# Kernel optimization log

Measured on AMD Instinct MI355X. Metric: run time of the kernel, lower is better.

Reference implementation:

```python
import jax, jax.numpy as jnp
import numpy as np

N_HEADS = 16
D_HEAD = 64
D_MODEL = 1024
CHUNK = 64
SCALE = 1.0 / np.sqrt(D_HEAD).astype(np.float32)


def binarize(x):
    # {-1,+1} with straight-through gradient (identity in bwd)
    return x + jax.lax.stop_gradient(jnp.where(x >= 0, 1.0, -1.0).astype(x.dtype) - x)


def setup_inputs() -> dict:
    key = jax.random.key(0)
    k1, k2, k3 = jax.random.split(key, 3)
    B, T, D = 2, 4096, D_MODEL
    x = jax.random.normal(k1, (B, T, D), dtype=jnp.float32)
    w_qkv = jax.random.normal(k2, (3 * D, D), dtype=jnp.float32) * (1.0 / np.sqrt(D))
    w_o = jax.random.normal(k3, (D, D), dtype=jnp.float32) * (1.0 / np.sqrt(D))
    return {"x": x, "w_qkv": w_qkv, "w_o": w_o}


def reference(x, w_qkv, w_o):
    B, T, D = x.shape
    H, d, C = N_HEADS, D_HEAD, CHUNK
    qkv = (x @ w_qkv.T).reshape(B, T, 3, H, d)
    q, k, v = qkv[:, :, 0], qkv[:, :, 1], qkv[:, :, 2]
    # -> (B, H, T, d)
    q = jnp.transpose(q, (0, 2, 1, 3)) * jnp.asarray(SCALE, x.dtype)
    k = binarize(jnp.transpose(k, (0, 2, 1, 3)))
    v = binarize(jnp.transpose(v, (0, 2, 1, 3)))

    assert T % C == 0  # T=4096 divisible by chunk=64 (pad branch not exercised)
    Nc = T // C
    qc = q.reshape(B, H, Nc, C, d)
    kc = k.reshape(B, H, Nc, C, d)
    vc = v.reshape(B, H, Nc, C, d)

    causal_mask = jnp.tril(jnp.ones((C, C), dtype=x.dtype))
    # intra-chunk: (B,H,N,C,C) scores, causal-masked, times values
    intra_scores = jnp.einsum('bhnid,bhnjd->bhnij', qc, kc) * causal_mask
    intra = jnp.einsum('bhnij,bhnjd->bhnid', intra_scores, vc)
    # per-chunk KV outer-product state: (B,H,N,d,d)
    chunk_kv = jnp.einsum('bhntk,bhntv->bhnkv', kc, vc)
    prefix = jnp.cumsum(chunk_kv, axis=2) - chunk_kv  # exclusive prefix
    cross = jnp.einsum('bhnck,bhnkv->bhncv', qc, prefix)
    output = (intra + cross).reshape(B, H, T, d)

    final_state = prefix[:, :, -1] + chunk_kv[:, :, -1]
    out = jnp.transpose(output, (0, 2, 1, 3)).reshape(B, T, D)
    return out @ w_o.T, final_state
```

## Files before the change

### kernel.cpp

```cpp
#include <hip/hip_runtime.h>

typedef __bf16 bf16;
typedef __bf16 bf16x8 __attribute__((ext_vector_type(8)));
typedef _Float16 f16;
typedef _Float16 f16x8 __attribute__((ext_vector_type(8)));
typedef float f32x4 __attribute__((ext_vector_type(4)));
typedef short s16x8 __attribute__((ext_vector_type(8)));

#define SCALE 0.125f
#define AP 72
#define CT 128

__device__ __forceinline__ void async_ld16(const void* g, void* l) {
  __builtin_amdgcn_global_load_lds((const __attribute__((address_space(1))) void*)g,
                                   (__attribute__((address_space(3))) void*)l, 16, 0, 0);
}

__global__ __launch_bounds__(256) void k_convert(
    const float* __restrict__ x, const float* __restrict__ wqkv, const float* __restrict__ wo,
    bf16* __restrict__ xsplit, bf16* __restrict__ wsplit, f16* __restrict__ wo16)
{
  const int N1 = 2097152, N2 = 786432, N3 = 262144;
  const int i = blockIdx.x * 256 + threadIdx.x;
  if (i < N1) {
    f32x4 v = ((const f32x4*)x)[i];
    int e = i * 4, m = e >> 10, c = e & 1023;
    bf16 hi[4], lo[4];
#pragma unroll
    for (int u = 0; u < 4; ++u) { hi[u] = (bf16)v[u]; lo[u] = (bf16)(v[u] - (float)hi[u]); }
    *(ulong1*)&xsplit[(size_t)m * 2048 + c] = *(ulong1*)hi;
    *(ulong1*)&xsplit[(size_t)m * 2048 + 1024 + c] = *(ulong1*)lo;
  } else if (i < N1 + N2) {
    int j = i - N1;
    f32x4 v = ((const f32x4*)wqkv)[j];
    int e = j * 4, n = e >> 10, c = e & 1023;
    bf16 hi[4], lo[4];
#pragma unroll
    for (int u = 0; u < 4; ++u) { hi[u] = (bf16)v[u]; lo[u] = (bf16)(v[u] - (float)hi[u]); }
    *(ulong1*)&wsplit[(size_t)n * 2048 + c] = *(ulong1*)hi;
    *(ulong1*)&wsplit[(size_t)n * 2048 + 1024 + c] = *(ulong1*)lo;
  } else if (i < N1 + N2 + N3) {
    int j = i - N1 - N2;
    f32x4 v = ((const f32x4*)wo)[j];
    f16 h[4];
#pragma unroll
    for (int u = 0; u < 4; ++u) h[u] = (f16)v[u];
    *(ulong1*)&wo16[(size_t)j * 4] = *(ulong1*)h;
  }
}

__global__ __launch_bounds__(256) void k_gemm_qkv(
    const bf16* __restrict__ A, const bf16* __restrict__ B,
    bf16* __restrict__ Qws, bf16* __restrict__ Kws, bf16* __restrict__ Vws)
{
  __shared__ char smem[32768];
  const int tid = threadIdx.x;
  const int wave = tid >> 6, lane = tid & 63;
  const int quad = lane >> 4, l16 = lane & 15;
  const int bxr = (blockIdx.x < 16) ? (blockIdx.x + 8) : (blockIdx.x - 16);
  const int n0 = bxr * 128;
  const int m0 = blockIdx.y * 128;
  const int wm = (wave >> 1) << 6, wn = (wave & 1) << 6;
  const int region = n0 >> 10;
  f32x4 acc[4][4] = {};

  if (region == 0) {
    bf16* As = (bf16*)smem;
    bf16* Bs = As + 128 * 64;
    const int r8 = lane >> 3, c8 = lane & 7;
    const int sw = l16 & 7;
    const int srcoff = (c8 ^ r8) * 8;
    for (int k0 = 0; k0 < 1024; k0 += 64) {
      __syncthreads();
#pragma unroll
      for (int it = 0; it < 4; ++it) {
        const int row = wave * 32 + it * 8 + r8;
        async_ld16(A + (size_t)(m0 + row) * 2048 + k0 + srcoff, As + row * 64 + c8 * 8);
        async_ld16(B + (size_t)(n0 + row) * 2048 + k0 + srcoff, Bs + row * 64 + c8 * 8);
      }
      __syncthreads();
#pragma unroll
      for (int ks = 0; ks < 64; ks += 32) {
        bf16x8 af[4], bg[4];
#pragma unroll
        for (int mi = 0; mi < 4; ++mi)
          af[mi] = *(const bf16x8*)&As[(wm + mi * 16 + l16) * 64 + ((((ks >> 3) + quad) ^ sw) << 3)];
#pragma unroll
        for (int ni = 0; ni < 4; ++ni)
          bg[ni] = *(const bf16x8*)&Bs[(wn + ni * 16 + l16) * 64 + ((((ks >> 3) + quad) ^ sw) << 3)];
#pragma unroll
        for (int mi = 0; mi < 4; ++mi)
#pragma unroll
          for (int ni = 0; ni < 4; ++ni)
            acc[mi][ni] = __builtin_amdgcn_mfma_f32_16x16x32_bf16(af[mi], bg[ni], acc[mi][ni], 0, 0, 0);
      }
    }
  } else {
    bf16* Ah = (bf16*)smem;
    bf16* Al = Ah + 128 * 32;
    bf16* Bh = Al + 128 * 32;
    bf16* Bl = Bh + 128 * 32;
    const int rr0 = tid >> 2;
    const int sl = tid & 3;
    const int rsw = quad ^ ((l16 >> 1) & 3);
    for (int k0 = 0; k0 < 1024; k0 += 32) {
      __syncthreads();
#pragma unroll
      for (int rr = 0; rr < 2; ++rr) {
        const int row = rr * 64 + rr0;
        const int soff = ((sl ^ ((row >> 1) & 3)) << 3);
        const bf16* arow = A + (size_t)(m0 + row) * 2048 + k0 + soff;
        const bf16* brow = B + (size_t)(n0 + row) * 2048 + k0 + soff;
        async_ld16(arow,        Ah + row * 32 + sl * 8);
        async_ld16(arow + 1024, Al + row * 32 + sl * 8);
        async_ld16(brow,        Bh + row * 32 + sl * 8);
        async_ld16(brow + 1024, Bl + row * 32 + sl * 8);
      }
      __syncthreads();
#pragma unroll
      for (int cb = 0; cb < 3; ++cb) {
        const bf16* Asrc = (cb == 1) ? Al : Ah;
        const bf16* Bsrc = (cb == 2) ? Bl : Bh;
        bf16x8 af[4], bg[4];
#pragma unroll
        for (int mi = 0; mi < 4; ++mi)
          af[mi] = *(const bf16x8*)&Asrc[(wm + mi * 16 + l16) * 32 + (rsw << 3)];
#pragma unroll
        for (int ni = 0; ni < 4; ++ni)
          bg[ni] = *(const bf16x8*)&Bsrc[(wn + ni * 16 + l16) * 32 + (rsw << 3)];
#pragma unroll
        for (int mi = 0; mi < 4; ++mi)
#pragma unroll
          for (int ni = 0; ni < 4; ++ni)
            acc[mi][ni] = __builtin_amdgcn_mfma_f32_16x16x32_bf16(af[mi], bg[ni], acc[mi][ni], 0, 0, 0);
      }
    }
  }

  bf16* Ct = (bf16*)smem;
  __syncthreads();
#pragma unroll
  for (int mi = 0; mi < 4; ++mi) {
    const int ml = wm + mi * 16 + quad * 4;
#pragma unroll
    for (int ni = 0; ni < 4; ++ni) {
      const int nl = wn + ni * 16 + l16;
#pragma unroll
      for (int r = 0; r < 4; ++r) {
        const float v = acc[mi][ni][r];
        bf16 o;
        if (region == 0) o = (bf16)(v * SCALE);
        else             o = (bf16)((v >= 0.f) ? 1.f : -1.f);
        Ct[(ml + r) * CT + nl] = o;
      }
    }
  }
  __syncthreads();
  {
    const int row = tid >> 1, half = tid & 1;
    const int nn = (n0 & 1023) + half * 64;
    const int h = nn >> 6;
    const int b = m0 >> 12, t = (m0 & 4095) + row;
    bf16* base = (region == 0) ? Qws : (region == 1) ? Kws : Vws;
    bf16* dst = base + ((size_t)(b * 16 + h) * 4096 + t) * 64;
    const bf16* src = &Ct[row * CT + half * 64];
#pragma unroll
    for (int u = 0; u < 8; ++u)
      *(bf16x8*)(dst + u * 8) = *(const bf16x8*)(src + u * 8);
  }
}

__global__ __launch_bounds__(256) void k_ckv(
    const bf16* __restrict__ Kws, const bf16* __restrict__ Vws, short* __restrict__ ckv)
{
  __shared__ bf16 Kt[64 * AP];
  __shared__ bf16 Vt[64 * AP];
  const int tid = threadIdx.x;
  const int nchunk = blockIdx.x & 63, bh = blockIdx.x >> 6;
  const size_t tbase = ((size_t)bh * 4096 + (size_t)nchunk * 64) * 64;
  const int row = tid >> 2, c0 = (tid & 3) << 4;
  {
    const bf16x8* gk = (const bf16x8*)(Kws + tbase + row * 64 + c0);
    const bf16x8* gv = (const bf16x8*)(Vws + tbase + row * 64 + c0);
    bf16x8 k0 = gk[0], k1 = gk[1], v0 = gv[0], v1 = gv[1];
#pragma unroll
    for (int u = 0; u < 8; ++u) {
      Kt[(c0 + u) * AP + row] = k0[u];
      Kt[(c0 + 8 + u) * AP + row] = k1[u];
      Vt[(c0 + u) * AP + row] = v0[u];
      Vt[(c0 + 8 + u) * AP + row] = v1[u];
    }
  }
  __syncthreads();
  const int wave = tid >> 6, lane = tid & 63;
  const int quad = lane >> 4, l16 = lane & 15;
  const int ti = wave;
  bf16x8 ka[2];
#pragma unroll
  for (int kk = 0; kk < 2; ++kk)
    ka[kk] = *(const bf16x8*)&Kt[(ti * 16 + l16) * AP + kk * 32 + quad * 8];
  short* dst = ckv + ((size_t)bh * 64 + nchunk) * 4096;
#pragma unroll
  for (int td = 0; td < 4; ++td) {
    f32x4 acc = {};
#pragma unroll
    for (int kk = 0; kk < 2; ++kk) {
      const bf16x8 vb = *(const bf16x8*)&Vt[(td * 16 + l16) * AP + kk * 32 + quad * 8];
      acc = __builtin_amdgcn_mfma_f32_16x16x32_bf16(ka[kk], vb, acc, 0, 0, 0);
    }
#pragma unroll
    for (int r = 0; r < 4; ++r)
      dst[(ti * 16 + quad * 4 + r) * 64 + td * 16 + l16] = (short)acc[r];
  }
}

__global__ __launch_bounds__(256) void k_scan(short* __restrict__ ckv, float* __restrict__ fin)
{
  const int idx2 = blockIdx.x * 256 + threadIdx.x;
  short* p = ckv + ((size_t)(idx2 >> 11)) * 262144 + (size_t)(idx2 & 2047) * 2;
  int r0 = 0, r1 = 0;
#pragma unroll
  for (int n = 0; n < 64; ++n) {
    unsigned int w = *(unsigned int*)(p + (size_t)n * 4096);
    const short a = (short)(w & 0xffff);
    const short bb = (short)(w >> 16);
    *(unsigned int*)(p + (size_t)n * 4096) =
        ((unsigned int)(unsigned short)(short)r0) | (((unsigned int)(unsigned short)(short)r1) << 16);
    r0 += a; r1 += bb;
  }
  float2 f; f.x = (float)r0; f.y = (float)r1;
  *(float2*)(fin + ((size_t)(idx2 >> 11)) * 4096 + (size_t)(idx2 & 2047) * 2) = f;
}

__global__ __launch_bounds__(256) void k_attn(
    const bf16* __restrict__ Qws, const bf16* __restrict__ Kws, const bf16* __restrict__ Vws,
    const short* __restrict__ pref, f16* __restrict__ attn)
{
  __shared__ bf16 Ks[64 * 64];
  __shared__ bf16 Vt[64 * AP];
  __shared__ bf16 Ph[64 * AP];
  __shared__ bf16 Pl[64 * AP];
  __shared__ bf16 Ss[64 * AP];
  const int tid = threadIdx.x;
  const int nchunk = blockIdx.x & 63, bh = blockIdx.x >> 6;
  const int b = bh >> 4, h = bh & 15;
  const size_t tbase = ((size_t)bh * 4096 + (size_t)nchunk * 64) * 64;

  {
    const int c8 = tid & 7, r0 = tid >> 3;
#pragma unroll
    for (int it = 0; it < 2; ++it) {
      const int row = it * 32 + r0;
      async_ld16(Kws + tbase + row * 64 + ((c8 ^ (row & 7)) << 3), Ks + row * 64 + (c8 << 3));
    }
  }
  const int wave = tid >> 6, lane = tid & 63;
  const int quad = lane >> 4, l16 = lane & 15;
  const int ti = wave;
  bf16x8 qa[2];
#pragma unroll
  for (int kk = 0; kk < 2; ++kk)
    qa[kk] = *(const bf16x8*)(Qws + tbase + (ti * 16 + l16) * 64 + kk * 32 + quad * 8);
  {
    const int row = tid >> 2, c0 = (tid & 3) << 4;
    const bf16x8* gv = (const bf16x8*)(Vws + tbase + row * 64 + c0);
    bf16x8 v0 = gv[0], v1 = gv[1];
#pragma unroll
    for (int u = 0; u < 8; ++u) {
      Vt[(c0 + u) * AP + row] = v0[u];
      Vt[(c0 + 8 + u) * AP + row] = v1[u];
    }
    const short* gp = pref + ((size_t)bh * 64 + nchunk) * 4096 + row * 64 + c0;
    s16x8 p0 = *(const s16x8*)(gp);
    s16x8 p1 = *(const s16x8*)(gp + 8);
#pragma unroll
    for (int u = 0; u < 8; ++u) {
      {
        const float p = (float)p0[u];
        const bf16 hi = (bf16)p;
        Ph[(c0 + u) * AP + row] = hi;
        Pl[(c0 + u) * AP + row] = (bf16)(p - (float)hi);
      }
      {
        const float p = (float)p1[u];
        const bf16 hi = (bf16)p;
        Ph[(c0 + 8 + u) * AP + row] = hi;
        Pl[(c0 + 8 + u) * AP + row] = (bf16)(p - (float)hi);
      }
    }
  }
  __syncthreads();

  const int sw = l16 & 7;
  f32x4 sacc[4] = {};
#pragma unroll
  for (int tj = 0; tj < 4; ++tj)
#pragma unroll
    for (int kk = 0; kk < 2; ++kk) {
      const bf16x8 kb = *(const bf16x8*)&Ks[(tj * 16 + l16) * 64 + (((kk * 4 + quad) ^ sw) << 3)];
      sacc[tj] = __builtin_amdgcn_mfma_f32_16x16x32_bf16(qa[kk], kb, sacc[tj], 0, 0, 0);
    }
#pragma unroll
  for (int tj = 0; tj < 4; ++tj)
#pragma unroll
    for (int r = 0; r < 4; ++r) {
      const int i = ti * 16 + quad * 4 + r;
      const int jj = tj * 16 + l16;
      Ss[i * AP + jj] = (bf16)((jj <= i) ? sacc[tj][r] : 0.f);
    }
  __syncthreads();

  bf16x8 sa[2];
#pragma unroll
  for (int kk = 0; kk < 2; ++kk)
    sa[kk] = *(const bf16x8*)&Ss[(ti * 16 + l16) * AP + kk * 32 + quad * 8];
  f32x4 oacc[4] = {};
#pragma unroll
  for (int td = 0; td < 4; ++td) {
#pragma unroll
    for (int kk = 0; kk < 2; ++kk) {
      const bf16x8 vb = *(const bf16x8*)&Vt[(td * 16 + l16) * AP + kk * 32 + quad * 8];
      oacc[td] = __builtin_amdgcn_mfma_f32_16x16x32_bf16(sa[kk], vb, oacc[td], 0, 0, 0);
    }
#pragma unroll
    for (int kk = 0; kk < 2; ++kk) {
      const bf16x8 pb = *(const bf16x8*)&Ph[(td * 16 + l16) * AP + kk * 32 + quad * 8];
      oacc[td] = __builtin_amdgcn_mfma_f32_16x16x32_bf16(qa[kk], pb, oacc[td], 0, 0, 0);
      const bf16x8 pb2 = *(const bf16x8*)&Pl[(td * 16 + l16) * AP + kk * 32 + quad * 8];
      oacc[td] = __builtin_amdgcn_mfma_f32_16x16x32_bf16(qa[kk], pb2, oacc[td], 0, 0, 0);
    }
  }
  __syncthreads();
  f16* Os = (f16*)Ss;
#pragma unroll
  for (int td = 0; td < 4; ++td)
#pragma unroll
    for (int r = 0; r < 4; ++r) {
      const int i = ti * 16 + quad * 4 + r;
      const int dd = td * 16 + l16;
      Os[i * AP + dd] = (f16)oacc[td][r];
    }
  __syncthreads();
  {
    const int i2 = tid >> 2, q4 = tid & 3;
    const int t = nchunk * 64 + i2;
    f16* dst = attn + ((size_t)(b * 4096 + t)) * 1024 + h * 64 + q4 * 16;
    const f16* src = &Os[i2 * AP + q4 * 16];
    *(f16x8*)(dst) = *(const f16x8*)(src);
    *(f16x8*)(dst + 8) = *(const f16x8*)(src + 8);
  }
}

__global__ __launch_bounds__(256) void k_gemm_out(
    const f16* __restrict__ A, const f16* __restrict__ B, float* __restrict__ out)
{
  __shared__ f16 As[128 * 64];
  __shared__ f16 Bs[128 * 64];
  const int tid = threadIdx.x;
  const int wave = tid >> 6, lane = tid & 63;
  const int quad = lane >> 4, l16 = lane & 15;
  const int n0 = blockIdx.x * 128;
  const int m0 = blockIdx.y * 128;
  const int wm = (wave >> 1) << 6, wn = (wave & 1) << 6;
  const int r8 = lane >> 3, c8 = lane & 7;
  const int sw = l16 & 7;
  const int srcoff = (c8 ^ r8) * 8;
  f32x4 acc[4][4] = {};

  for (int k0 = 0; k0 < 1024; k0 += 64) {
    __syncthreads();
#pragma unroll
    for (int it = 0; it < 4; ++it) {
      const int row = wave * 32 + it * 8 + r8;
      async_ld16(A + (size_t)(m0 + row) * 1024 + k0 + srcoff, As + row * 64 + c8 * 8);
      async_ld16(B + (size_t)(n0 + row) * 1024 + k0 + srcoff, Bs + row * 64 + c8 * 8);
    }
    __syncthreads();
#pragma unroll
    for (int ks = 0; ks < 64; ks += 32) {
      f16x8 af[4], bg[4];
#pragma unroll
      for (int mi = 0; mi < 4; ++mi)
        af[mi] = *(const f16x8*)&As[(wm + mi * 16 + l16) * 64 + ((((ks >> 3) + quad) ^ sw) << 3)];
#pragma unroll
      for (int ni = 0; ni < 4; ++ni)
        bg[ni] = *(const f16x8*)&Bs[(wn + ni * 16 + l16) * 64 + ((((ks >> 3) + quad) ^ sw) << 3)];
#pragma unroll
      for (int mi = 0; mi < 4; ++mi)
#pragma unroll
        for (int ni = 0; ni < 4; ++ni)
          acc[mi][ni] = __builtin_amdgcn_mfma_f32_16x16x32_f16(af[mi], bg[ni], acc[mi][ni], 0, 0, 0);
    }
  }
#pragma unroll
  for (int mi = 0; mi < 4; ++mi)
#pragma unroll
    for (int ni = 0; ni < 4; ++ni)
#pragma unroll
      for (int r = 0; r < 4; ++r) {
        const int m = m0 + wm + mi * 16 + quad * 4 + r;
        const int n = n0 + wn + ni * 16 + l16;
        out[(size_t)m * 1024 + n] = acc[mi][ni][r];
      }
}

extern "C" void kernel_launch(void* const* d_in, const int* in_sizes, int n_in,
                              void* d_out, int out_size, void* d_ws, size_t ws_size,
                              hipStream_t stream)
{
  const float* x = (const float*)d_in[0];
  const float* wqkv = (const float*)d_in[1];
  const float* wo = (const float*)d_in[2];
  float* out = (float*)d_out;
  char* ws = (char*)d_ws;

  bf16* xsplit = (bf16*)(ws);
  bf16* wsplit = (bf16*)(ws + 33554432);
  f16*  wo16   = (f16*)(ws + 46137344);
  bf16* Qws    = (bf16*)(ws + 48234496);
  bf16* Kws    = (bf16*)(ws + 65011712);
  bf16* Vws    = (bf16*)(ws + 81788928);
  short* ckv   = (short*)(ws + 98566144);
  f16*  attn   = (f16*)(ws + 132120576);
  float* fin   = out + 8388608;

  k_convert<<<12288, 256, 0, stream>>>(x, wqkv, wo, xsplit, wsplit, wo16);
  k_gemm_qkv<<<dim3(24, 64), 256, 0, stream>>>(xsplit, wsplit, Qws, Kws, Vws);
  k_ckv<<<2048, 256, 0, stream>>>(Kws, Vws, ckv);
  k_scan<<<256, 256, 0, stream>>>(ckv, fin);
  k_attn<<<2048, 256, 0, stream>>>(Qws, Kws, Vws, ckv, attn);
  k_gemm_out<<<dim3(8, 64), 256, 0, stream>>>(attn, wo16, out);
}
```

Before: 285.3 us.

## Rewrite QKV GEMM as 256x256 8-wave kernel with double-buffered async staging

Replaces the 128x128, 4-wave QKV GEMM with a 256x256-tile, 512-thread kernel. It double-buffers A and B in 128 KB of dynamic LDS, interleaves async global-to-LDS loads with MFMA phases, and uses s_setprio and explicit vmcnt waits to overlap loading with compute. The split-bf16 K/V path becomes a single 48-step loop whose k index wraps to form the hi*hi, lo*hi and hi*lo products. Q blocks take 16 steps and K/V blocks 48, all in one flat grid. The aim is more operand reuse per loaded byte and hidden load latency. The cost is heavy LDS use that limits occupancy to one block per CU, plus uneven block lengths between the Q and K/V regions.

```diff
diff --git a/kernel.cpp b/kernel.cpp
--- a/kernel.cpp
+++ b/kernel.cpp
@@ -9,7 +9,6 @@
 
 #define SCALE 0.125f
 #define AP 72
-#define CT 128
 
 __device__ __forceinline__ void async_ld16(const void* g, void* l) {
   __builtin_amdgcn_global_load_lds((const __attribute__((address_space(1))) void*)g,
@@ -49,124 +48,204 @@
   }
 }
 
-__global__ __launch_bounds__(256) void k_gemm_qkv(
+#define STAGE_HALF(gptr, lptr, orig, koff)                                                   \
+  {                                                                                          \
+    const int i0_ = tid;                                                                     \
+    const int r0_ = i0_ >> 3, c0_ = i0_ & 7;                                                 \
+    async_ld16((gptr) + (size_t)((orig) + r0_) * 2048 + (koff) + ((c0_ ^ (r0_ & 7)) << 3),   \
+               (lptr) + i0_ * 8);                                                            \
+    const int i1_ = 512 + tid;                                                               \
+    const int r1_ = i1_ >> 3, c1_ = i1_ & 7;                                                 \
+    async_ld16((gptr) + (size_t)((orig) + r1_) * 2048 + (koff) + ((c1_ ^ (r1_ & 7)) << 3),   \
+               (lptr) + i1_ * 8);                                                            \
+  }
+
+#define LDA_FRAG(dst, Ab, fr, ks)                                                            \
+  dst = *(const bf16x8*)&(Ab)[((wm << 7) + ((fr) << 4) + l16) * 64 +                         \
+                              (((((ks) << 2) + quad) ^ sw7) << 3)];
+
+#define LDB_FRAG(dst, Bb, n, ks)                                                             \
+  dst = *(const bf16x8*)&(Bb)[((wn << 6) + ((n) << 4) + l16) * 64 +                          \
+                              (((((ks) << 2) + quad) ^ sw7) << 3)];
+
+#define PH_READA(q, Ab)                                                                      \
+  bf16x8 af00, af01, af10, af11;                                                             \
+  LDA_FRAG(af00, Ab, 2 * (q), 0);                                                            \
+  LDA_FRAG(af01, Ab, 2 * (q), 1);                                                            \
+  LDA_FRAG(af10, Ab, 2 * (q) + 1, 0);                                                        \
+  LDA_FRAG(af11, Ab, 2 * (q) + 1, 1);
+
+#define PH_READB(Bb)                                                                         \
+  LDB_FRAG(bg[0][0], Bb, 0, 0); LDB_FRAG(bg[1][0], Bb, 1, 0);                                \
+  LDB_FRAG(bg[2][0], Bb, 2, 0); LDB_FRAG(bg[3][0], Bb, 3, 0);                                \
+  LDB_FRAG(bg[0][1], Bb, 0, 1); LDB_FRAG(bg[1][1], Bb, 1, 1);                                \
+  LDB_FRAG(bg[2][1], Bb, 2, 1); LDB_FRAG(bg[3][1], Bb, 3, 1);
+
+#define MFMA_Q(q)                                                                            \
+  acc[2*(q)  ][0] = __builtin_amdgcn_mfma_f32_16x16x32_bf16(af00, bg[0][0], acc[2*(q)  ][0], 0, 0, 0); \
+  acc[2*(q)  ][1] = __builtin_amdgcn_mfma_f32_16x16x32_bf16(af00, bg[1][0], acc[2*(q)  ][1], 0, 0, 0); \
+  acc[2*(q)  ][2] = __builtin_amdgcn_mfma_f32_16x16x32_bf16(af00, bg[2][0], acc[2*(q)  ][2], 0, 0, 0); \
+  acc[2*(q)  ][3] = __builtin_amdgcn_mfma_f32_16x16x32_bf16(af00, bg[3][0], acc[2*(q)  ][3], 0, 0, 0); \
+  acc[2*(q)+1][0] = __builtin_amdgcn_mfma_f32_16x16x32_bf16(af10, bg[0][0], acc[2*(q)+1][0], 0, 0, 0); \
+  acc[2*(q)+1][1] = __builtin_amdgcn_mfma_f32_16x16x32_bf16(af10, bg[1][0], acc[2*(q)+1][1], 0, 0, 0); \
+  acc[2*(q)+1][2] = __builtin_amdgcn_mfma_f32_16x16x32_bf16(af10, bg[2][0], acc[2*(q)+1][2], 0, 0, 0); \
+  acc[2*(q)+1][3] = __builtin_amdgcn_mfma_f32_16x16x32_bf16(af10, bg[3][0], acc[2*(q)+1][3], 0, 0, 0); \
+  acc[2*(q)  ][0] = __builtin_amdgcn_mfma_f32_16x16x32_bf16(af01, bg[0][1], acc[2*(q)  ][0], 0, 0, 0); \
+  acc[2*(q)  ][1] = __builtin_amdgcn_mfma_f32_16x16x32_bf16(af01, bg[1][1], acc[2*(q)  ][1], 0, 0, 0); \
+  acc[2*(q)  ][2] = __builtin_amdgcn_mfma_f32_16x16x32_bf16(af01, bg[2][1], acc[2*(q)  ][2], 0, 0, 0); \
+  acc[2*(q)  ][3] = __builtin_amdgcn_mfma_f32_16x16x32_bf16(af01, bg[3][1], acc[2*(q)  ][3], 0, 0, 0); \
+  acc[2*(q)+1][0] = __builtin_amdgcn_mfma_f32_16x16x32_bf16(af11, bg[0][1], acc[2*(q)+1][0], 0, 0, 0); \
+  acc[2*(q)+1][1] = __builtin_amdgcn_mfma_f32_16x16x32_bf16(af11, bg[1][1], acc[2*(q)+1][1], 0, 0, 0); \
+  acc[2*(q)+1][2] = __builtin_amdgcn_mfma_f32_16x16x32_bf16(af11, bg[2][1], acc[2*(q)+1][2], 0, 0, 0); \
+  acc[2*(q)+1][3] = __builtin_amdgcn_mfma_f32_16x16x32_bf16(af11, bg[3][1], acc[2*(q)+1][3], 0, 0, 0);
+
+#define PH_MID()                                                                             \
+  __builtin_amdgcn_s_barrier();                                                              \
+  asm volatile("s_waitcnt lgkmcnt(0)" ::: "memory");                                         \
+  __builtin_amdgcn_s_setprio(1);
+
+#define PH_END()                                                                             \
+  __builtin_amdgcn_s_setprio(0);                                                             \
+  __builtin_amdgcn_s_barrier();
+
+#define PH_END_VM4()                                                                         \
+  __builtin_amdgcn_s_setprio(0);                                                             \
+  asm volatile("s_waitcnt vmcnt(4)" ::: "memory");                                           \
+  __builtin_amdgcn_s_barrier();                                                              \
+  asm volatile("" ::: "memory");
+
+__global__ __launch_bounds__(512, 2) void k_gemm_qkv8(
     const bf16* __restrict__ A, const bf16* __restrict__ B,
     bf16* __restrict__ Qws, bf16* __restrict__ Kws, bf16* __restrict__ Vws)
 {
-  __shared__ char smem[32768];
+  extern __shared__ bf16 smem[];
+  bf16* sA0 = smem;
+  bf16* sA1 = smem + 16384;
+  bf16* sB0 = smem + 32768;
+  bf16* sB1 = smem + 49152;
   const int tid = threadIdx.x;
-  const int wave = tid >> 6, lane = tid & 63;
+  const int lane = tid & 63;
+  const int wid = tid >> 6;
+  const int wm = wid >> 2, wn = wid & 3;
   const int quad = lane >> 4, l16 = lane & 15;
-  const int bxr = (blockIdx.x < 16) ? (blockIdx.x + 8) : (blockIdx.x - 16);
-  const int n0 = bxr * 128;
-  const int m0 = blockIdx.y * 128;
-  const int wm = (wave >> 1) << 6, wn = (wave & 1) << 6;
-  const int region = n0 >> 10;
-  f32x4 acc[4][4] = {};
-
-  if (region == 0) {
-    bf16* As = (bf16*)smem;
-    bf16* Bs = As + 128 * 64;
-    const int r8 = lane >> 3, c8 = lane & 7;
-    const int sw = l16 & 7;
-    const int srcoff = (c8 ^ r8) * 8;
-    for (int k0 = 0; k0 < 1024; k0 += 64) {
-      __syncthreads();
-#pragma unroll
-      for (int it = 0; it < 4; ++it) {
-        const int row = wave * 32 + it * 8 + r8;
-        async_ld16(A + (size_t)(m0 + row) * 2048 + k0 + srcoff, As + row * 64 + c8 * 8);
-        async_ld16(B + (size_t)(n0 + row) * 2048 + k0 + srcoff, Bs + row * 64 + c8 * 8);
-      }
-      __syncthreads();
-#pragma unroll
-      for (int ks = 0; ks < 64; ks += 32) {
-        bf16x8 af[4], bg[4];
-#pragma unroll
-        for (int mi = 0; mi < 4; ++mi)
-          af[mi] = *(const bf16x8*)&As[(wm + mi * 16 + l16) * 64 + ((((ks >> 3) + quad) ^ sw) << 3)];
-#pragma unroll
-        for (int ni = 0; ni < 4; ++ni)
-          bg[ni] = *(const bf16x8*)&Bs[(wn + ni * 16 + l16) * 64 + ((((ks >> 3) + quad) ^ sw) << 3)];
-#pragma unroll
-        for (int mi = 0; mi < 4; ++mi)
-#pragma unroll
-          for (int ni = 0; ni < 4; ++ni)
-            acc[mi][ni] = __builtin_amdgcn_mfma_f32_16x16x32_bf16(af[mi], bg[ni], acc[mi][ni], 0, 0, 0);
-      }
-    }
-  } else {
-    bf16* Ah = (bf16*)smem;
-    bf16* Al = Ah + 128 * 32;
-    bf16* Bh = Al + 128 * 32;
-    bf16* Bl = Bh + 128 * 32;
-    const int rr0 = tid >> 2;
-    const int sl = tid & 3;
-    const int rsw = quad ^ ((l16 >> 1) & 3);
-    for (int k0 = 0; k0 < 1024; k0 += 32) {
-      __syncthreads();
-#pragma unroll
-      for (int rr = 0; rr < 2; ++rr) {
-        const int row = rr * 64 + rr0;
-        const int soff = ((sl ^ ((row >> 1) & 3)) << 3);
-        const bf16* arow = A + (size_t)(m0 + row) * 2048 + k0 + soff;
-        const bf16* brow = B + (size_t)(n0 + row) * 2048 + k0 + soff;
-        async_ld16(arow,        Ah + row * 32 + sl * 8);
-        async_ld16(arow + 1024, Al + row * 32 + sl * 8);
-        async_ld16(brow,        Bh + row * 32 + sl * 8);
-        async_ld16(brow + 1024, Bl + row * 32 + sl * 8);
-      }
-      __syncthreads();
-#pragma unroll
-      for (int cb = 0; cb < 3; ++cb) {
-        const bf16* Asrc = (cb == 1) ? Al : Ah;
-        const bf16* Bsrc = (cb == 2) ? Bl : Bh;
-        bf16x8 af[4], bg[4];
-#pragma unroll
-        for (int mi = 0; mi < 4; ++mi)
-          af[mi] = *(const bf16x8*)&Asrc[(wm + mi * 16 + l16) * 32 + (rsw << 3)];
-#pragma unroll
-        for (int ni = 0; ni < 4; ++ni)
-          bg[ni] = *(const bf16x8*)&Bsrc[(wn + ni * 16 + l16) * 32 + (rsw << 3)];
-#pragma unroll
-        for (int mi = 0; mi < 4; ++mi)
-#pragma unroll
-          for (int ni = 0; ni < 4; ++ni)
-            acc[mi][ni] = __builtin_amdgcn_mfma_f32_16x16x32_bf16(af[mi], bg[ni], acc[mi][ni], 0, 0, 0);
-      }
-    }
-  }
-
-  bf16* Ct = (bf16*)smem;
-  __syncthreads();
-#pragma unroll
-  for (int mi = 0; mi < 4; ++mi) {
-    const int ml = wm + mi * 16 + quad * 4;
-#pragma unroll
-    for (int ni = 0; ni < 4; ++ni) {
-      const int nl = wn + ni * 16 + l16;
-#pragma unroll
-      for (int r = 0; r < 4; ++r) {
-        const float v = acc[mi][ni][r];
-        bf16 o;
-        if (region == 0) o = (bf16)(v * SCALE);
-        else             o = (bf16)((v >= 0.f) ? 1.f : -1.f);
-        Ct[(ml + r) * CT + nl] = o;
-      }
-    }
-  }
-  __syncthreads();
+  const int sw7 = l16 & 7;
+
+  const int bid = blockIdx.x;
+  const bool isQ = bid >= 256;
+  int mb, nb, NT;
+  if (isQ) { mb = (bid - 256) >> 2; nb = (bid - 256) & 3; NT = 16; }
+  else     { mb = bid >> 3;         nb = bid & 7;         NT = 48; }
+  const int m0 = mb << 8;
+  const int n0 = nb << 8;
+  const int Bor = isQ ? n0 : (1024 + n0);
+
+  f32x4 acc[8][4] = {};
+  bf16x8 bg[4][2];
+
+  STAGE_HALF(A, sA0, m0, 0);
+  asm volatile("" ::: "memory");
+  STAGE_HALF(A, sA0 + 8192, m0 + 128, 0);
+  asm volatile("" ::: "memory");
+  STAGE_HALF(B, sB0, Bor, 0);
+  asm volatile("" ::: "memory");
+  STAGE_HALF(B, sB0 + 8192, Bor + 128, 0);
+  asm volatile("" ::: "memory");
+  STAGE_HALF(B, sB1, Bor, 64);
+  asm volatile("" ::: "memory");
+  STAGE_HALF(B, sB1 + 8192, Bor + 128, 64);
+  asm volatile("s_waitcnt vmcnt(4)" ::: "memory");
+  __builtin_amdgcn_s_barrier();
+  asm volatile("" ::: "memory");
+
+  for (int kt = 0; kt < NT; kt += 2) {
+    const int t2 = (kt + 2 < NT) ? (kt + 2) : (kt + 2 - NT);
+    const int t3 = (kt + 3 < NT) ? (kt + 3) : (kt + 3 - NT);
+    const int ka1 = (isQ ? (kt + 1) : ((kt + 1) < 32 ? (kt + 1) : (kt + 1 - 32))) << 6;
+    const int ka2 = (isQ ? t2 : (t2 < 32 ? t2 : t2 - 32)) << 6;
+    const int kb2 = (isQ ? t2 : (t2 < 16 ? t2 : t2 - 16)) << 6;
+    const int kb3 = (isQ ? t3 : (t3 < 16 ? t3 : t3 - 16)) << 6;
+
+    {
+      PH_READA(0, sA0);
+      PH_READB(sB0);
+      STAGE_HALF(A, sA1, m0, ka1);
+      PH_MID(); MFMA_Q(0); PH_END();
+    }
+    {
+      PH_READA(1, sA0);
+      STAGE_HALF(A, sA1 + 8192, m0 + 128, ka1);
+      PH_MID(); MFMA_Q(1); PH_END();
+    }
+    {
+      PH_READA(2, sA0);
+      STAGE_HALF(B, sB0, Bor, kb2);
+      PH_MID(); MFMA_Q(2); PH_END();
+    }
+    {
+      PH_READA(3, sA0);
+      STAGE_HALF(B, sB0 + 8192, Bor + 128, kb2);
+      PH_MID(); MFMA_Q(3); PH_END_VM4();
+    }
+    {
+      PH_READA(0, sA1);
+      PH_READB(sB1);
+      STAGE_HALF(A, sA0, m0, ka2);
+      PH_MID(); MFMA_Q(0); PH_END();
+    }
+    {
+      PH_READA(1, sA1);
+      STAGE_HALF(A, sA0 + 8192, m0 + 128, ka2);
+      PH_MID(); MFMA_Q(1); PH_END();
+    }
+    {
+      PH_READA(2, sA1);
+      STAGE_HALF(B, sB1, Bor, kb3);
+      PH_MID(); MFMA_Q(2); PH_END();
+    }
+    {
+      PH_READA(3, sA1);
+      STAGE_HALF(B, sB1 + 8192, Bor + 128, kb3);
+      PH_MID(); MFMA_Q(3); PH_END_VM4();
+    }
+  }
+
+  asm volatile("s_waitcnt vmcnt(0)" ::: "memory");
+  __syncthreads();
+
   {
-    const int row = tid >> 1, half = tid & 1;
-    const int nn = (n0 & 1023) + half * 64;
-    const int h = nn >> 6;
-    const int b = m0 >> 12, t = (m0 & 4095) + row;
-    bf16* base = (region == 0) ? Qws : (region == 1) ? Kws : Vws;
-    bf16* dst = base + ((size_t)(b * 16 + h) * 4096 + t) * 64;
-    const bf16* src = &Ct[row * CT + half * 64];
-#pragma unroll
-    for (int u = 0; u < 8; ++u)
-      *(bf16x8*)(dst + u * 8) = *(const bf16x8*)(src + u * 8);
+    bf16* Ct = smem;
+#pragma unroll
+    for (int fr = 0; fr < 8; ++fr)
+#pragma unroll
+      for (int n = 0; n < 4; ++n)
+#pragma unroll
+        for (int r = 0; r < 4; ++r) {
+          const int row = (wm << 7) + (fr << 4) + (quad << 2) + r;
+          const int col = (wn << 6) + (n << 4) + l16;
+          const float v = acc[fr][n][r];
+          const bf16 o = isQ ? (bf16)(v * SCALE) : (bf16)((v >= 0.f) ? 1.f : -1.f);
+          Ct[row * 256 + ((((col >> 3) ^ (row & 7)) << 3) | (col & 7))] = o;
+        }
+  }
+  __syncthreads();
+  {
+    const int r2 = tid >> 1, hf = tid & 1;
+    const int mrow = m0 + r2;
+    const int bI = mrow >> 12, tI = mrow & 4095;
+#pragma unroll
+    for (int g = 0; g < 16; ++g) {
+      const int col = (hf << 7) + (g << 3);
+      const bf16x8 v8 = *(const bf16x8*)&smem[r2 * 256 + ((((col >> 3) ^ (r2 & 7)) << 3))];
+      const int gc = n0 + col;
+      bf16* dst;
+      if (isQ)
+        dst = Qws + ((size_t)(bI * 16 + (gc >> 6)) * 4096 + tI) * 64 + (gc & 63);
+      else if (gc < 1024)
+        dst = Kws + ((size_t)(bI * 16 + (gc >> 6)) * 4096 + tI) * 64 + (gc & 63);
+      else
+        dst = Vws + ((size_t)(bI * 16 + ((gc - 1024) >> 6)) * 4096 + tI) * 64 + ((gc - 1024) & 63);
+      *(bf16x8*)dst = v8;
+    }
   }
 }
 
@@ -425,7 +504,7 @@
   float* fin   = out + 8388608;
 
   k_convert<<<12288, 256, 0, stream>>>(x, wqkv, wo, xsplit, wsplit, wo16);
-  k_gemm_qkv<<<dim3(24, 64), 256, 0, stream>>>(xsplit, wsplit, Qws, Kws, Vws);
+  k_gemm_qkv8<<<dim3(384), 512, 131072, stream>>>(xsplit, wsplit, Qws, Kws, Vws);
   k_ckv<<<2048, 256, 0, stream>>>(Kws, Vws, ckv);
   k_scan<<<256, 256, 0, stream>>>(ckv, fin);
   k_attn<<<2048, 256, 0, stream>>>(Qws, Kws, Vws, ckv, attn);
```

New measurement: 290.5 us. Within noise of the previous version (+1.8%).
